# Kernel optimization log

Measured on AMD Instinct MI355X. Metric: run time of the kernel, lower is better.

## Reference

```python
import jax, jax.numpy as jnp
import numpy as np

D_IN = 1024
D_OUT = 1024
H = 16


def setup_inputs() -> dict:
    key = jax.random.key(0)
    ks = jax.random.split(key, 11)
    B, Tq, Tk = 2, 2048, 2048
    s = 1.0 / np.sqrt(D_IN)
    return {
        "q": jax.random.normal(ks[0], (B, Tq, D_IN), jnp.float32),
        "k": jax.random.normal(ks[1], (B, Tk, D_IN), jnp.float32),
        "v": jax.random.normal(ks[2], (B, Tk, D_IN), jnp.float32),
        "Wq": jax.random.uniform(ks[3], (D_IN, D_OUT), jnp.float32, -s, s),
        "bq": jax.random.uniform(ks[4], (D_OUT,), jnp.float32, -s, s),
        "Wk": jax.random.uniform(ks[5], (D_IN, D_OUT), jnp.float32, -s, s),
        "bk": jax.random.uniform(ks[6], (D_OUT,), jnp.float32, -s, s),
        "Wv": jax.random.uniform(ks[7], (D_IN, D_OUT), jnp.float32, -s, s),
        "bv": jax.random.uniform(ks[8], (D_OUT,), jnp.float32, -s, s),
        "Wo": jax.random.uniform(ks[9], (D_OUT, D_OUT), jnp.float32, -s, s),
        "bo": jax.random.uniform(ks[10], (D_OUT,), jnp.float32, -s, s),
    }


def reference(q, k, v, Wq, bq, Wk, bk, Wv, bv, Wo, bo):
    B, Tq, _ = q.shape
    Tk = k.shape[1]
    hd = D_OUT // H
    # QKV projections, split heads -> [B, H, T, hd]
    qh = (q @ Wq + bq).reshape(B, Tq, H, hd).transpose(0, 2, 1, 3)
    kh = (k @ Wk + bk).reshape(B, Tk, H, hd).transpose(0, 2, 1, 3)
    vh = (v @ Wv + bv).reshape(B, Tk, H, hd).transpose(0, 2, 1, 3)
    # scaled dot-product attention (scale uses key dim = head_dim)
    scores = jnp.einsum("bhqd,bhkd->bhqk", qh, kh) / jnp.sqrt(jnp.float32(hd))
    attn = jax.nn.softmax(scores, axis=-1)
    x = jnp.einsum("bhqk,bhkd->bhqd", attn, vh)
    x = x.transpose(0, 2, 1, 3).reshape(B, Tq, D_OUT)
    return x @ Wo + bo
```

## Files before the change

### kernel.cpp

```cpp
#include <hip/hip_runtime.h>
#include <hip/hip_bf16.h>

typedef __attribute__((ext_vector_type(8))) short short8;
typedef __attribute__((ext_vector_type(4))) short short4v;
typedef __attribute__((ext_vector_type(4))) float f32x4;

__device__ __forceinline__ unsigned short f2bf(float f) {
    __hip_bfloat16 h = __float2bfloat16(f);
    unsigned short u;
    __builtin_memcpy(&u, &h, 2);
    return u;
}
__device__ __forceinline__ short4v pack4bf(float a, float b, float c, float d) {
    union { __hip_bfloat162 h[2]; short4v s; } r;
    r.h[0] = __float22bfloat162_rn(make_float2(a, b));
    r.h[1] = __float22bfloat162_rn(make_float2(c, d));
    return r.s;
}

#define GLD16(gp, lp) __builtin_amdgcn_global_load_lds( \
    (const __attribute__((address_space(1))) void*)(gp), \
    (__attribute__((address_space(3))) void*)(lp), 16, 0, 0)

__global__ __launch_bounds__(256) void prep(
    const float* __restrict__ q, const float* __restrict__ k, const float* __restrict__ v,
    unsigned short* __restrict__ qb, unsigned short* __restrict__ kb, unsigned short* __restrict__ vb,
    const float* __restrict__ W0, const float* __restrict__ W1,
    const float* __restrict__ W2, const float* __restrict__ W3,
    unsigned short* __restrict__ T0, unsigned short* __restrict__ T1,
    unsigned short* __restrict__ T2, unsigned short* __restrict__ T3)
{
    __shared__ unsigned short Ts[64 * 72];
    int bx = blockIdx.x;
    if (bx < 6144) {
        const float* src; unsigned short* dst;
        switch (bx >> 11) { case 0: src = q; dst = qb; break;
                            case 1: src = k; dst = kb; break;
                            default: src = v; dst = vb; break; }
        size_t i = ((size_t)(bx & 2047) * 256 + threadIdx.x) * 8;
        float4 x0 = *(const float4*)&src[i];
        float4 x1 = *(const float4*)&src[i + 4];
        union { unsigned short s[8]; uint4 u; } p;
        p.s[0] = f2bf(x0.x); p.s[1] = f2bf(x0.y); p.s[2] = f2bf(x0.z); p.s[3] = f2bf(x0.w);
        p.s[4] = f2bf(x1.x); p.s[5] = f2bf(x1.y); p.s[6] = f2bf(x1.z); p.s[7] = f2bf(x1.w);
        *(uint4*)&dst[i] = p.u;
        return;
    }
    int w = bx - 6144;
    int z = w >> 8, rem = w & 255;
    int kx = rem >> 4, ny = rem & 15;
    const float* W;
    unsigned short* T;
    switch (z) {
        case 0: W = W0; T = T0; break;
        case 1: W = W1; T = T1; break;
        case 2: W = W2; T = T2; break;
        default: W = W3; T = T3; break;
    }
    int tid = threadIdx.x;
    int c = tid & 7, r = tid >> 3;
    int k0 = kx * 64, n0 = ny * 64;
    for (int i = 0; i < 64; i += 32) {
        const float* src = &W[(size_t)(k0 + r + i) * 1024 + n0 + c * 8];
        float4 x0 = *(const float4*)src;
        float4 x1 = *(const float4*)(src + 4);
        unsigned short* d = &Ts[(r + i) * 72 + c * 8];
        d[0] = f2bf(x0.x); d[1] = f2bf(x0.y); d[2] = f2bf(x0.z); d[3] = f2bf(x0.w);
        d[4] = f2bf(x1.x); d[5] = f2bf(x1.y); d[6] = f2bf(x1.z); d[7] = f2bf(x1.w);
    }
    __syncthreads();
    for (int i = 0; i < 64; i += 32) {
        union { unsigned short s[8]; uint4 v; } u;
        for (int j = 0; j < 8; j++) u.s[j] = Ts[(c * 8 + j) * 72 + (r + i)];
        *(uint4*)&T[(size_t)(n0 + r + i) * 1024 + k0 + c * 8] = u.v;
    }
}

__device__ __forceinline__ void gemm128_core(
    const unsigned short* __restrict__ A, const unsigned short* __restrict__ BT,
    const float* __restrict__ bias, unsigned short* __restrict__ out16,
    int mode, float scale)
{
    const int K = 1024;
    __shared__ unsigned short As[128 * 64];
    __shared__ unsigned short Bs[128 * 64];
    int tid = threadIdx.x;
    int m0 = blockIdx.x * 128, n0 = blockIdx.y * 128;
    int lane = tid & 63, wave = tid >> 6;
    int lm = lane & 15, quad = lane >> 4;
    int wm = (wave >> 1) * 64, wn = (wave & 1) * 64;

    int lrow = lane >> 3;
    int scol = ((lane & 7) ^ lrow) * 8;
    const unsigned short* Ag = A + (size_t)(m0 + wave * 32 + lrow) * K + scol;
    const unsigned short* Bg = BT + (size_t)(n0 + wave * 32 + lrow) * K + scol;
    unsigned short* AsW = &As[(wave * 32) * 64];
    unsigned short* BsW = &Bs[(wave * 32) * 64];

    f32x4 acc[4][4];
    for (int i = 0; i < 4; i++)
        for (int j = 0; j < 4; j++)
            for (int r = 0; r < 4; r++) acc[i][j][r] = 0.0f;

    for (int kb = 0; kb < K; kb += 64) {
        GLD16(Ag,          AsW);
        GLD16(Ag +  8 * K, AsW +  8 * 64);
        GLD16(Ag + 16 * K, AsW + 16 * 64);
        GLD16(Ag + 24 * K, AsW + 24 * 64);
        GLD16(Bg,          BsW);
        GLD16(Bg +  8 * K, BsW +  8 * 64);
        GLD16(Bg + 16 * K, BsW + 16 * 64);
        GLD16(Bg + 24 * K, BsW + 24 * 64);
        Ag += 64; Bg += 64;
        __syncthreads();
#pragma unroll
        for (int kk = 0; kk < 2; kk++) {
            int rp = ((kk * 4 + quad) ^ (lm & 7)) * 8;
            short8 a[4], b[4];
            for (int i = 0; i < 4; i++)
                a[i] = *(const short8*)&As[(wm + i * 16 + lm) * 64 + rp];
            for (int j = 0; j < 4; j++)
                b[j] = *(const short8*)&Bs[(wn + j * 16 + lm) * 64 + rp];
            for (int i = 0; i < 4; i++)
                for (int j = 0; j < 4; j++)
                    acc[i][j] = __builtin_amdgcn_mfma_f32_16x16x32_bf16(a[i], b[j], acc[i][j], 0, 0, 0);
        }
        __syncthreads();
    }

    for (int j = 0; j < 4; j++) {
        int col = n0 + wn + j * 16 + lm;
        float bv = bias[col];
        for (int i = 0; i < 4; i++) {
            int rowb = m0 + wm + i * 16 + quad * 4;
            int h = col >> 6, d = col & 63;
            int bb = rowb >> 11, t = rowb & 2047;
            if (mode == 1) {
                size_t base = (((size_t)(bb * 16 + h)) * 2048 + t) * 64 + d;
                for (int r = 0; r < 4; r++)
                    out16[base + (size_t)r * 64] = f2bf((acc[i][j][r] + bv) * scale);
            } else {
                ushort4 pk;
                pk.x = f2bf((acc[i][j][0] + bv) * scale);
                pk.y = f2bf((acc[i][j][1] + bv) * scale);
                pk.z = f2bf((acc[i][j][2] + bv) * scale);
                pk.w = f2bf((acc[i][j][3] + bv) * scale);
                *(ushort4*)&out16[(((size_t)(bb * 16 + h)) * 64 + d) * 2048 + t] = pk;
            }
        }
    }
}

__global__ __launch_bounds__(256, 3) void qkv_gemm(
    const unsigned short* __restrict__ qbf, const unsigned short* __restrict__ kbf,
    const unsigned short* __restrict__ vbf,
    const unsigned short* __restrict__ WqT, const unsigned short* __restrict__ WkT,
    const unsigned short* __restrict__ WvT,
    const float* __restrict__ bq, const float* __restrict__ bk, const float* __restrict__ bv,
    unsigned short* __restrict__ Qh, unsigned short* __restrict__ Kh,
    unsigned short* __restrict__ VhT)
{
    switch (blockIdx.z) {
        case 0:  gemm128_core(qbf, WqT, bq, Qh,  1, 0.18033688011f); break;
        case 1:  gemm128_core(kbf, WkT, bk, Kh,  1, 1.0f);           break;
        default: gemm128_core(vbf, WvT, bv, VhT, 2, 1.0f);           break;
    }
}

__global__ __launch_bounds__(256, 2) void out_gemm(
    const unsigned short* __restrict__ A, const unsigned short* __restrict__ BT,
    const float* __restrict__ bias, float* __restrict__ out)
{
    const int K = 1024;
    __shared__ unsigned short As[128 * 64];
    __shared__ unsigned short Bs[64 * 64];
    int tid = threadIdx.x;
    int m0 = blockIdx.x * 128, n0 = blockIdx.y * 64;
    int lane = tid & 63, wave = tid >> 6;
    int lm = lane & 15, quad = lane >> 4;
    int wm = wave * 32;

    int lrow = lane >> 3;
    int scol = ((lane & 7) ^ lrow) * 8;
    const unsigned short* Ag = A + (size_t)(m0 + wave * 32 + lrow) * K + scol;
    const unsigned short* Bg = BT + (size_t)(n0 + wave * 16 + lrow) * K + scol;
    unsigned short* AsW = &As[(wave * 32) * 64];
    unsigned short* BsW = &Bs[(wave * 16) * 64];

    f32x4 acc[2][4];
    for (int i = 0; i < 2; i++)
        for (int j = 0; j < 4; j++)
            for (int r = 0; r < 4; r++) acc[i][j][r] = 0.0f;

    for (int kb = 0; kb < K; kb += 64) {
        GLD16(Ag,          AsW);
        GLD16(Ag +  8 * K, AsW +  8 * 64);
        GLD16(Ag + 16 * K, AsW + 16 * 64);
        GLD16(Ag + 24 * K, AsW + 24 * 64);
        GLD16(Bg,          BsW);
        GLD16(Bg +  8 * K, BsW +  8 * 64);
        Ag += 64; Bg += 64;
        __syncthreads();
#pragma unroll
        for (int kk = 0; kk < 2; kk++) {
            int rp = ((kk * 4 + quad) ^ (lm & 7)) * 8;
            short8 a[2], b[4];
            for (int i = 0; i < 2; i++)
                a[i] = *(const short8*)&As[(wm + i * 16 + lm) * 64 + rp];
            for (int j = 0; j < 4; j++)
                b[j] = *(const short8*)&Bs[(j * 16 + lm) * 64 + rp];
            for (int i = 0; i < 2; i++)
                for (int j = 0; j < 4; j++)
                    acc[i][j] = __builtin_amdgcn_mfma_f32_16x16x32_bf16(a[i], b[j], acc[i][j], 0, 0, 0);
        }
        __syncthreads();
    }

    for (int j = 0; j < 4; j++) {
        int col = n0 + j * 16 + lm;
        float bv = bias[col];
        for (int i = 0; i < 2; i++) {
            int rowb = m0 + wm + i * 16 + quad * 4;
            for (int r = 0; r < 4; r++)
                out[(size_t)(rowb + r) * 1024 + col] = acc[i][j][r] + bv;
        }
    }
}

__global__ __launch_bounds__(256) void attn_kernel(
    const unsigned short* __restrict__ Qh, const unsigned short* __restrict__ Kh,
    const unsigned short* __restrict__ VhT, unsigned short* __restrict__ X)
{
    __shared__ unsigned short Ks[4][64 * 64];
    __shared__ unsigned short Vt[4][64 * 64];

    int tid = threadIdx.x;
    int qblk = blockIdx.x & 15, bh = blockIdx.x >> 4;
    int b = bh >> 4, h = bh & 15;
    int lane = tid & 63, wave = tid >> 6;
    int lm = lane & 15, quad = lane >> 4;

    const unsigned short* Kbase = Kh + (size_t)bh * 2048 * 64;
    const unsigned short* Vbase = VhT + (size_t)bh * 64 * 2048;

    int srow = wave * 8 + (lane >> 3);
    int schk = ((lane & 7) ^ ((lane >> 3) & 7)) * 8;
    int swz  = lm & 7;

    const char* ks0 = (const char*)&Ks[0][0] + lm * 128 + ((quad ^ swz) * 16);
    const char* ks1 = (const char*)&Ks[0][0] + lm * 128 + (((quad + 4) ^ swz) * 16);
    int qh2 = quad >> 1, wo = (quad & 1) * 8;
    const char* vt0 = (const char*)&Vt[0][0] + lm * 128 + (((0 + qh2) ^ swz) * 16) + wo;
    const char* vt1 = (const char*)&Vt[0][0] + lm * 128 + (((2 + qh2) ^ swz) * 16) + wo;
    const char* vt2 = (const char*)&Vt[0][0] + lm * 128 + (((4 + qh2) ^ swz) * 16) + wo;
    const char* vt3 = (const char*)&Vt[0][0] + lm * 128 + (((6 + qh2) ^ swz) * 16) + wo;

    const unsigned short* Kg = Kbase + (size_t)srow * 64 + schk;
    const unsigned short* Vg = Vbase + (size_t)srow * 2048 + schk;

    int qrow = qblk * 128 + wave * 32 + lm;
    const unsigned short* qptr = Qh + ((size_t)bh * 2048 + qrow) * 64;
    short8 qfa0 = *(const short8*)&qptr[quad * 8];
    short8 qfa1 = *(const short8*)&qptr[32 + quad * 8];
    short8 qfb0 = *(const short8*)&qptr[16 * 64 + quad * 8];
    short8 qfb1 = *(const short8*)&qptr[16 * 64 + 32 + quad * 8];
    asm volatile("s_waitcnt vmcnt(0)" ::: "memory");

    f32x4 oA[4], oB[4];
    for (int n = 0; n < 4; n++)
        for (int r = 0; r < 4; r++) { oA[n][r] = 0.0f; oB[n][r] = 0.0f; }
    float lA = 0.0f, lB = 0.0f;
    f32x4 zf;
    zf[0] = zf[1] = zf[2] = zf[3] = 0.0f;

#define STAGE(BUF) do { \
        GLD16(Kg,             &Ks[BUF][(wave * 8) * 64]); \
        GLD16(Kg + 32 * 64,   &Ks[BUF][(32 + wave * 8) * 64]); \
        GLD16(Vg,             &Vt[BUF][(wave * 8) * 64]); \
        GLD16(Vg + 32 * 2048, &Vt[BUF][(32 + wave * 8) * 64]); \
        Kg += 64 * 64; Vg += 64; } while (0)

#define PHASE(WAITN) do { \
        asm volatile("s_waitcnt vmcnt(" #WAITN ")" ::: "memory"); \
        __builtin_amdgcn_s_barrier(); \
        asm volatile("" ::: "memory"); \
        __builtin_amdgcn_sched_barrier(0); } while (0)

#define QKPV(CUR) do { \
        short4v pa[4], pb[4]; \
        _Pragma("unroll") \
        for (int t = 0; t < 4; t++) { \
            short8 ka0 = *(const short8*)(ks0 + (CUR) * 8192 + t * 2048); \
            short8 ka1 = *(const short8*)(ks1 + (CUR) * 8192 + t * 2048); \
            f32x4 za = __builtin_amdgcn_mfma_f32_16x16x32_bf16(ka0, qfa0, zf, 0, 0, 0); \
            za = __builtin_amdgcn_mfma_f32_16x16x32_bf16(ka1, qfa1, za, 0, 0, 0); \
            f32x4 zb = __builtin_amdgcn_mfma_f32_16x16x32_bf16(ka0, qfb0, zf, 0, 0, 0); \
            zb = __builtin_amdgcn_mfma_f32_16x16x32_bf16(ka1, qfb1, zb, 0, 0, 0); \
            float a0 = __builtin_amdgcn_exp2f(za[0]); \
            float a1 = __builtin_amdgcn_exp2f(za[1]); \
            float a2 = __builtin_amdgcn_exp2f(za[2]); \
            float a3 = __builtin_amdgcn_exp2f(za[3]); \
            lA += (a0 + a1) + (a2 + a3); \
            pa[t] = pack4bf(a0, a1, a2, a3); \
            float b0 = __builtin_amdgcn_exp2f(zb[0]); \
            float b1 = __builtin_amdgcn_exp2f(zb[1]); \
            float b2 = __builtin_amdgcn_exp2f(zb[2]); \
            float b3 = __builtin_amdgcn_exp2f(zb[3]); \
            lB += (b0 + b1) + (b2 + b3); \
            pb[t] = pack4bf(b0, b1, b2, b3); \
        } \
        _Pragma("unroll") \
        for (int n = 0; n < 4; n++) { \
            short4v v0 = *(const short4v*)(vt0 + (CUR) * 8192 + n * 2048); \
            short4v v1 = *(const short4v*)(vt1 + (CUR) * 8192 + n * 2048); \
            short4v v2 = *(const short4v*)(vt2 + (CUR) * 8192 + n * 2048); \
            short4v v3 = *(const short4v*)(vt3 + (CUR) * 8192 + n * 2048); \
            oA[n] = __builtin_amdgcn_mfma_f32_16x16x16bf16_1k(pa[0], v0, oA[n], 0, 0, 0); \
            oB[n] = __builtin_amdgcn_mfma_f32_16x16x16bf16_1k(pb[0], v0, oB[n], 0, 0, 0); \
            oA[n] = __builtin_amdgcn_mfma_f32_16x16x16bf16_1k(pa[1], v1, oA[n], 0, 0, 0); \
            oB[n] = __builtin_amdgcn_mfma_f32_16x16x16bf16_1k(pb[1], v1, oB[n], 0, 0, 0); \
            oA[n] = __builtin_amdgcn_mfma_f32_16x16x16bf16_1k(pa[2], v2, oA[n], 0, 0, 0); \
            oB[n] = __builtin_amdgcn_mfma_f32_16x16x16bf16_1k(pb[2], v2, oB[n], 0, 0, 0); \
            oA[n] = __builtin_amdgcn_mfma_f32_16x16x16bf16_1k(pa[3], v3, oA[n], 0, 0, 0); \
            oB[n] = __builtin_amdgcn_mfma_f32_16x16x16bf16_1k(pb[3], v3, oB[n], 0, 0, 0); \
        } } while (0)

    STAGE(0); STAGE(1); STAGE(2);

    for (int u = 0; u < 7; u++) {
        PHASE(8); STAGE(3); QKPV(0);
        PHASE(8); STAGE(0); QKPV(1);
        PHASE(8); STAGE(1); QKPV(2);
        PHASE(8); STAGE(2); QKPV(3);
    }
    PHASE(8); STAGE(3); QKPV(0);
    PHASE(8); QKPV(1);
    PHASE(4); QKPV(2);
    PHASE(0); QKPV(3);

#undef STAGE
#undef PHASE
#undef QKPV

    lA += __shfl_xor(lA, 16);
    lA += __shfl_xor(lA, 32);
    lB += __shfl_xor(lB, 16);
    lB += __shfl_xor(lB, 32);
    float invA = 1.0f / lA;
    float invB = 1.0f / lB;

    for (int r = 0; r < 4; r++) {
        int src = (lane & 48) | (quad * 4 + r);
        float invAr = __shfl(invA, src);
        float invBr = __shfl(invB, src);
        int rowA = qblk * 128 + wave * 32 + quad * 4 + r;
        for (int n = 0; n < 4; n++) {
            X[((size_t)b * 2048 + rowA) * 1024 + h * 64 + n * 16 + lm] = f2bf(oA[n][r] * invAr);
            X[((size_t)b * 2048 + rowA + 16) * 1024 + h * 64 + n * 16 + lm] = f2bf(oB[n][r] * invBr);
        }
    }
}

extern "C" void kernel_launch(void* const* d_in, const int* in_sizes, int n_in,
                              void* d_out, int out_size, void* d_ws, size_t ws_size,
                              hipStream_t stream)
{
    const float* q  = (const float*)d_in[0];
    const float* k  = (const float*)d_in[1];
    const float* v  = (const float*)d_in[2];
    const float* Wq = (const float*)d_in[3];
    const float* bq = (const float*)d_in[4];
    const float* Wk = (const float*)d_in[5];
    const float* bk = (const float*)d_in[6];
    const float* Wv = (const float*)d_in[7];
    const float* bv = (const float*)d_in[8];
    const float* Wo = (const float*)d_in[9];
    const float* bo = (const float*)d_in[10];

    unsigned short* ws  = (unsigned short*)d_ws;
    const unsigned int M1 = 1u << 20;
    unsigned short* WqT = ws;
    unsigned short* WkT = ws + M1;
    unsigned short* WvT = ws + 2 * M1;
    unsigned short* WoT = ws + 3 * M1;
    unsigned short* qbf = ws + 4 * M1;
    unsigned short* kbf = ws + 8 * M1;
    unsigned short* vbf = ws + 12 * M1;
    unsigned short* Qh  = ws + 16 * M1;
    unsigned short* Kh  = ws + 4 * M1;
    unsigned short* VhT = ws + 8 * M1;
    unsigned short* X   = ws + 12 * M1;

    prep<<<dim3(7168), 256, 0, stream>>>(q, k, v, qbf, kbf, vbf,
                                         Wq, Wk, Wv, Wo, WqT, WkT, WvT, WoT);
    qkv_gemm<<<dim3(32, 8, 3), 256, 0, stream>>>(qbf, kbf, vbf, WqT, WkT, WvT,
                                                 bq, bk, bv, Qh, Kh, VhT);
    attn_kernel<<<dim3(512), 256, 0, stream>>>(Qh, Kh, VhT, X);
    out_gemm<<<dim3(32, 16), 256, 0, stream>>>(X, WoT, bo, (float*)d_out);
}
```

Baseline: 224.1 us.

## Triple-buffer LDS K-tiles in projection GEMMs with async global-to-LDS prefetch

Replaces the single-buffered 64-wide K loop in the QKV and output GEMMs with a three-stage ring of 32-wide K tiles. Global-to-LDS loads for future tiles are issued ahead of the MFMA work, and waits use vmcnt counts with one barrier per step. The aim is to hide global load latency and drop the second __syncthreads per iteration. In exchange it uses a new swizzle for 32-wide rows, slightly more LDS, and more barrier phases of smaller MFMA batches.

New measurement: 219.8 us. About the same (-1.9%).

```diff
diff --git a/kernel.cpp b/kernel.cpp
--- a/kernel.cpp
+++ b/kernel.cpp
@@ -21,6 +21,12 @@
 #define GLD16(gp, lp) __builtin_amdgcn_global_load_lds( \
     (const __attribute__((address_space(1))) void*)(gp), \
     (__attribute__((address_space(3))) void*)(lp), 16, 0, 0)
+
+#define PHASE(WAITN) do { \
+        asm volatile("s_waitcnt vmcnt(" #WAITN ")" ::: "memory"); \
+        __builtin_amdgcn_s_barrier(); \
+        asm volatile("" ::: "memory"); \
+        __builtin_amdgcn_sched_barrier(0); } while (0)
 
 __global__ __launch_bounds__(256) void prep(
     const float* __restrict__ q, const float* __restrict__ k, const float* __restrict__ v,
@@ -76,57 +82,65 @@
     }
 }
 
-__device__ __forceinline__ void gemm128_core(
+__device__ __forceinline__ void gemm_core_p(
     const unsigned short* __restrict__ A, const unsigned short* __restrict__ BT,
     const float* __restrict__ bias, unsigned short* __restrict__ out16,
     int mode, float scale)
 {
     const int K = 1024;
-    __shared__ unsigned short As[128 * 64];
-    __shared__ unsigned short Bs[128 * 64];
+    __shared__ unsigned short As[3][128 * 32];
+    __shared__ unsigned short Bs[3][128 * 32];
     int tid = threadIdx.x;
     int m0 = blockIdx.x * 128, n0 = blockIdx.y * 128;
     int lane = tid & 63, wave = tid >> 6;
     int lm = lane & 15, quad = lane >> 4;
     int wm = (wave >> 1) * 64, wn = (wave & 1) * 64;
 
-    int lrow = lane >> 3;
-    int scol = ((lane & 7) ^ lrow) * 8;
+    int lrow = lane >> 2;
+    int scol = ((lane & 3) ^ ((lane >> 3) & 3)) * 8;
     const unsigned short* Ag = A + (size_t)(m0 + wave * 32 + lrow) * K + scol;
     const unsigned short* Bg = BT + (size_t)(n0 + wave * 32 + lrow) * K + scol;
-    unsigned short* AsW = &As[(wave * 32) * 64];
-    unsigned short* BsW = &Bs[(wave * 32) * 64];
+
+    int rpos = (quad ^ ((lm >> 1) & 3)) * 8;
 
     f32x4 acc[4][4];
     for (int i = 0; i < 4; i++)
         for (int j = 0; j < 4; j++)
             for (int r = 0; r < 4; r++) acc[i][j][r] = 0.0f;
 
-    for (int kb = 0; kb < K; kb += 64) {
-        GLD16(Ag,          AsW);
-        GLD16(Ag +  8 * K, AsW +  8 * 64);
-        GLD16(Ag + 16 * K, AsW + 16 * 64);
-        GLD16(Ag + 24 * K, AsW + 24 * 64);
-        GLD16(Bg,          BsW);
-        GLD16(Bg +  8 * K, BsW +  8 * 64);
-        GLD16(Bg + 16 * K, BsW + 16 * 64);
-        GLD16(Bg + 24 * K, BsW + 24 * 64);
-        Ag += 64; Bg += 64;
-        __syncthreads();
-#pragma unroll
-        for (int kk = 0; kk < 2; kk++) {
-            int rp = ((kk * 4 + quad) ^ (lm & 7)) * 8;
-            short8 a[4], b[4];
-            for (int i = 0; i < 4; i++)
-                a[i] = *(const short8*)&As[(wm + i * 16 + lm) * 64 + rp];
-            for (int j = 0; j < 4; j++)
-                b[j] = *(const short8*)&Bs[(wn + j * 16 + lm) * 64 + rp];
-            for (int i = 0; i < 4; i++)
-                for (int j = 0; j < 4; j++)
-                    acc[i][j] = __builtin_amdgcn_mfma_f32_16x16x32_bf16(a[i], b[j], acc[i][j], 0, 0, 0);
-        }
-        __syncthreads();
-    }
+#define GSTAGE(BUF) do { \
+        GLD16(Ag,          &As[BUF][(wave * 32) * 32]); \
+        GLD16(Ag + 16 * K, &As[BUF][(wave * 32 + 16) * 32]); \
+        GLD16(Bg,          &Bs[BUF][(wave * 32) * 32]); \
+        GLD16(Bg + 16 * K, &Bs[BUF][(wave * 32 + 16) * 32]); \
+        Ag += 32; Bg += 32; } while (0)
+
+#define GCOMP(BUF) do { \
+        short8 a[4], b[4]; \
+        _Pragma("unroll") \
+        for (int i = 0; i < 4; i++) \
+            a[i] = *(const short8*)&As[BUF][(wm + i * 16 + lm) * 32 + rpos]; \
+        _Pragma("unroll") \
+        for (int j = 0; j < 4; j++) \
+            b[j] = *(const short8*)&Bs[BUF][(wn + j * 16 + lm) * 32 + rpos]; \
+        _Pragma("unroll") \
+        for (int i = 0; i < 4; i++) \
+            _Pragma("unroll") \
+            for (int j = 0; j < 4; j++) \
+                acc[i][j] = __builtin_amdgcn_mfma_f32_16x16x32_bf16(a[i], b[j], acc[i][j], 0, 0, 0); \
+        } while (0)
+
+    GSTAGE(0); GSTAGE(1);
+    for (int u = 0; u < 10; u++) {
+        PHASE(4); GSTAGE(2); GCOMP(0);
+        PHASE(4); GSTAGE(0); GCOMP(1);
+        PHASE(4); GSTAGE(1); GCOMP(2);
+    }
+    PHASE(4); GCOMP(0);
+    PHASE(0); GCOMP(1);
+
+#undef GSTAGE
+#undef GCOMP
 
     for (int j = 0; j < 4; j++) {
         int col = n0 + wn + j * 16 + lm;
@@ -161,9 +175,9 @@
     unsigned short* __restrict__ VhT)
 {
     switch (blockIdx.z) {
-        case 0:  gemm128_core(qbf, WqT, bq, Qh,  1, 0.18033688011f); break;
-        case 1:  gemm128_core(kbf, WkT, bk, Kh,  1, 1.0f);           break;
-        default: gemm128_core(vbf, WvT, bv, VhT, 2, 1.0f);           break;
+        case 0:  gemm_core_p(qbf, WqT, bq, Qh,  1, 0.18033688011f); break;
+        case 1:  gemm_core_p(kbf, WkT, bk, Kh,  1, 1.0f);           break;
+        default: gemm_core_p(vbf, WvT, bv, VhT, 2, 1.0f);           break;
     }
 }
 
@@ -172,49 +186,58 @@
     const float* __restrict__ bias, float* __restrict__ out)
 {
     const int K = 1024;
-    __shared__ unsigned short As[128 * 64];
-    __shared__ unsigned short Bs[64 * 64];
+    __shared__ unsigned short As[3][128 * 32];
+    __shared__ unsigned short Bs[3][64 * 32];
     int tid = threadIdx.x;
     int m0 = blockIdx.x * 128, n0 = blockIdx.y * 64;
     int lane = tid & 63, wave = tid >> 6;
     int lm = lane & 15, quad = lane >> 4;
     int wm = wave * 32;
 
-    int lrow = lane >> 3;
-    int scol = ((lane & 7) ^ lrow) * 8;
+    int lrow = lane >> 2;
+    int scol = ((lane & 3) ^ ((lane >> 3) & 3)) * 8;
     const unsigned short* Ag = A + (size_t)(m0 + wave * 32 + lrow) * K + scol;
     const unsigned short* Bg = BT + (size_t)(n0 + wave * 16 + lrow) * K + scol;
-    unsigned short* AsW = &As[(wave * 32) * 64];
-    unsigned short* BsW = &Bs[(wave * 16) * 64];
+
+    int rpos = (quad ^ ((lm >> 1) & 3)) * 8;
 
     f32x4 acc[2][4];
     for (int i = 0; i < 2; i++)
         for (int j = 0; j < 4; j++)
             for (int r = 0; r < 4; r++) acc[i][j][r] = 0.0f;
 
-    for (int kb = 0; kb < K; kb += 64) {
-        GLD16(Ag,          AsW);
-        GLD16(Ag +  8 * K, AsW +  8 * 64);
-        GLD16(Ag + 16 * K, AsW + 16 * 64);
-        GLD16(Ag + 24 * K, AsW + 24 * 64);
-        GLD16(Bg,          BsW);
-        GLD16(Bg +  8 * K, BsW +  8 * 64);
-        Ag += 64; Bg += 64;
-        __syncthreads();
-#pragma unroll
-        for (int kk = 0; kk < 2; kk++) {
-            int rp = ((kk * 4 + quad) ^ (lm & 7)) * 8;
-            short8 a[2], b[4];
-            for (int i = 0; i < 2; i++)
-                a[i] = *(const short8*)&As[(wm + i * 16 + lm) * 64 + rp];
-            for (int j = 0; j < 4; j++)
-                b[j] = *(const short8*)&Bs[(j * 16 + lm) * 64 + rp];
-            for (int i = 0; i < 2; i++)
-                for (int j = 0; j < 4; j++)
-                    acc[i][j] = __builtin_amdgcn_mfma_f32_16x16x32_bf16(a[i], b[j], acc[i][j], 0, 0, 0);
-        }
-        __syncthreads();
-    }
+#define OSTAGE(BUF) do { \
+        GLD16(Ag,          &As[BUF][(wave * 32) * 32]); \
+        GLD16(Ag + 16 * K, &As[BUF][(wave * 32 + 16) * 32]); \
+        GLD16(Bg,          &Bs[BUF][(wave * 16) * 32]); \
+        Ag += 32; Bg += 32; } while (0)
+
+#define OCOMP(BUF) do { \
+        short8 a[2], b[4]; \
+        _Pragma("unroll") \
+        for (int i = 0; i < 2; i++) \
+            a[i] = *(const short8*)&As[BUF][(wm + i * 16 + lm) * 32 + rpos]; \
+        _Pragma("unroll") \
+        for (int j = 0; j < 4; j++) \
+            b[j] = *(const short8*)&Bs[BUF][(j * 16 + lm) * 32 + rpos]; \
+        _Pragma("unroll") \
+        for (int i = 0; i < 2; i++) \
+            _Pragma("unroll") \
+            for (int j = 0; j < 4; j++) \
+                acc[i][j] = __builtin_amdgcn_mfma_f32_16x16x32_bf16(a[i], b[j], acc[i][j], 0, 0, 0); \
+        } while (0)
+
+    OSTAGE(0); OSTAGE(1);
+    for (int u = 0; u < 10; u++) {
+        PHASE(3); OSTAGE(2); OCOMP(0);
+        PHASE(3); OSTAGE(0); OCOMP(1);
+        PHASE(3); OSTAGE(1); OCOMP(2);
+    }
+    PHASE(3); OCOMP(0);
+    PHASE(0); OCOMP(1);
+
+#undef OSTAGE
+#undef OCOMP
 
     for (int j = 0; j < 4; j++) {
         int col = n0 + j * 16 + lm;
@@ -279,12 +302,6 @@
         GLD16(Vg,             &Vt[BUF][(wave * 8) * 64]); \
         GLD16(Vg + 32 * 2048, &Vt[BUF][(32 + wave * 8) * 64]); \
         Kg += 64 * 64; Vg += 64; } while (0)
-
-#define PHASE(WAITN) do { \
-        asm volatile("s_waitcnt vmcnt(" #WAITN ")" ::: "memory"); \
-        __builtin_amdgcn_s_barrier(); \
-        asm volatile("" ::: "memory"); \
-        __builtin_amdgcn_sched_barrier(0); } while (0)
 
 #define QKPV(CUR) do { \
         short4v pa[4], pb[4]; \
@@ -339,7 +356,6 @@
     PHASE(0); QKPV(3);
 
 #undef STAGE
-#undef PHASE
 #undef QKPV
 
     lA += __shfl_xor(lA, 16);
```
